# Kernel optimization log

Hardware: AMD Instinct MI355X
Metric: run time of the kernel (lower is better)

## Reference

```python
import jax, jax.numpy as jnp
import numpy as np


def setup_inputs() -> dict:
    key = jax.random.key(0)
    k1, k2 = jax.random.split(key)
    N = 16384
    NUM_ANCHORS = 64
    HIDDEN_DIM = 128
    adj = jax.random.uniform(k1, (N, N), dtype=jnp.float32)
    anchor_emb = jax.random.normal(k2, (NUM_ANCHORS, HIDDEN_DIM), dtype=jnp.float32)
    return {"adj": adj, "anchor_emb": anchor_emb}


def reference(adj, anchor_emb):
    # adj: [N, N], anchor_emb: [A, H]
    num_anchors = anchor_emb.shape[0]
    deg = jnp.sum(adj, axis=-1, keepdims=True)              # [N, 1]
    nrm = jnp.linalg.norm(deg) + 1e-6                       # scalar ||deg||_F
    # sim[:, :A] of (deg @ deg.T)/nrm computed directly without the full NxN product
    sim = (deg * deg[:num_anchors, 0][None, :]) / nrm       # [N, A]
    anchor_weights = jax.nn.softmax(sim, axis=-1)           # [N, A]
    return anchor_weights @ anchor_emb                      # [N, H]
```

## Files before the change

kernel.cpp:

```cpp
#include <hip/hip_runtime.h>


constexpr int N_NODES = 16384;
constexpr int N_ANCH  = 64;
constexpr int HID     = 128;
constexpr int ROWS_PER_BLOCK = 8;
constexpr int K1_BLOCKS = N_NODES / ROWS_PER_BLOCK;
constexpr int K3_BLOCKS = 1024;

typedef float f4 __attribute__((ext_vector_type(4)));

__global__ __launch_bounds__(256) void rowsum_kernel(const float* __restrict__ adj,
                                                     float* __restrict__ deg,
                                                     float* __restrict__ ssq_part) {
    const int t = threadIdx.x, lane = t & 63, wid = t >> 6;
    const int row0 = blockIdx.x * ROWS_PER_BLOCK + wid * 2;
    float ssq = 0.0f;

    for (int r = 0; r < 2; ++r) {
        const int row = row0 + r;
        const f4* __restrict__ p =
            reinterpret_cast<const f4*>(adj) + (size_t)row * (N_NODES / 4) + lane;
        float s = 0.0f;
        for (int c = 0; c < 4; ++c) {
            f4 v[16];
#pragma unroll
            for (int i = 0; i < 16; ++i)
                v[i] = __builtin_nontemporal_load(p + c * 1024 + i * 64);
#pragma unroll
            for (int i = 0; i < 16; ++i)
                s += (v[i].x + v[i].y) + (v[i].z + v[i].w);
        }
#pragma unroll
        for (int off = 32; off > 0; off >>= 1) s += __shfl_down(s, off, 64);
        if (lane == 0) { deg[row] = s; ssq = fmaf(s, s, ssq); }
    }

    __shared__ float sp[4];
    if (lane == 0) sp[wid] = ssq;
    __syncthreads();
    if (t == 0) ssq_part[blockIdx.x] = (sp[0] + sp[1]) + (sp[2] + sp[3]);
}

__global__ __launch_bounds__(256) void out_kernel(const float* __restrict__ deg,
                                                  const float* __restrict__ ssq_part,
                                                  const float* __restrict__ emb,
                                                  float* __restrict__ out) {
    __shared__ float s_emb[N_ANCH * HID];
    __shared__ float s_w[4][N_ANCH];
    __shared__ float s_red[4];
    __shared__ float s_inv;

    const int t = threadIdx.x, lane = t & 63, wid = t >> 6;

    float ss = 0.0f;
#pragma unroll
    for (int i = 0; i < K1_BLOCKS / 256; ++i) ss += ssq_part[t + i * 256];
#pragma unroll
    for (int off = 32; off > 0; off >>= 1) ss += __shfl_down(ss, off, 64);
    if (lane == 0) s_red[wid] = ss;

    for (int i = t; i < N_ANCH * HID / 4; i += 256)
        reinterpret_cast<f4*>(s_emb)[i] = reinterpret_cast<const f4*>(emb)[i];
    __syncthreads();
    if (t == 0)
        s_inv = 1.0f / (sqrtf((s_red[0] + s_red[1]) + (s_red[2] + s_red[3])) + 1e-6f);
    __syncthreads();
    const float inv_nrm = s_inv;

    float e0[N_ANCH], e1[N_ANCH];
#pragma unroll
    for (int a = 0; a < N_ANCH; ++a) {
        e0[a] = s_emb[a * HID + lane];
        e1[a] = s_emb[a * HID + 64 + lane];
    }

    const float da = deg[lane] * inv_nrm;
    const int row0 = (blockIdx.x * 4 + wid) * 4;

    for (int r = 0; r < 4; ++r) {
        const int row = row0 + r;
        const float sim = deg[row] * da;

        float m = sim;
#pragma unroll
        for (int off = 32; off > 0; off >>= 1) m = fmaxf(m, __shfl_xor(m, off, 64));
        const float e = __expf(sim - m);
        float sum = e;
#pragma unroll
        for (int off = 32; off > 0; off >>= 1) sum += __shfl_xor(sum, off, 64);
        s_w[wid][lane] = e / sum;

        float acc0 = 0.0f, acc1 = 0.0f;
#pragma unroll
        for (int a4 = 0; a4 < N_ANCH; a4 += 4) {
            f4 w4 = *reinterpret_cast<const f4*>(&s_w[wid][a4]);
            acc0 = fmaf(w4.x, e0[a4 + 0], acc0); acc1 = fmaf(w4.x, e1[a4 + 0], acc1);
            acc0 = fmaf(w4.y, e0[a4 + 1], acc0); acc1 = fmaf(w4.y, e1[a4 + 1], acc1);
            acc0 = fmaf(w4.z, e0[a4 + 2], acc0); acc1 = fmaf(w4.z, e1[a4 + 2], acc1);
            acc0 = fmaf(w4.w, e0[a4 + 3], acc0); acc1 = fmaf(w4.w, e1[a4 + 3], acc1);
        }
        out[(size_t)row * HID + lane]      = acc0;
        out[(size_t)row * HID + 64 + lane] = acc1;
    }
}

extern "C" void kernel_launch(void* const* d_in, const int* in_sizes, int n_in,
                              void* d_out, int out_size, void* d_ws, size_t ws_size,
                              hipStream_t stream) {
    const float* adj = (const float*)d_in[0];
    const float* emb = (const float*)d_in[1];
    float* out = (float*)d_out;

    float* deg      = (float*)d_ws;
    float* ssq_part = deg + N_NODES;

    rowsum_kernel<<<K1_BLOCKS, 256, 0, stream>>>(adj, deg, ssq_part);
    out_kernel<<<K3_BLOCKS, 256, 0, stream>>>(deg, ssq_part, emb, out);
}
```

Measured before the change: 180.7 us.

## Fuse rowsum and output kernels into one cooperative kernel with grid sync

Merges the row-sum/degree kernel and the softmax-weighted output kernel into a single cooperative launch of 512 blocks, with a grid-wide sync between the two phases. Each block now reads 32 rows of adj instead of 8, and the anchor embedding is staged into shared memory before the stream. The output phase splits work so each wave handles one 64-column half across 16 rows. This removes a kernel launch and its tail gap, at the cost of a grid barrier, fewer blocks for the bandwidth-bound adj stream, and a cooperative-launch residency requirement.

```diff
diff --git a/kernel.cpp b/kernel.cpp
--- a/kernel.cpp
+++ b/kernel.cpp
@@ -1,23 +1,36 @@
 #include <hip/hip_runtime.h>
+#include <hip/hip_cooperative_groups.h>
+
+namespace cg = cooperative_groups;
 
 
 constexpr int N_NODES = 16384;
 constexpr int N_ANCH  = 64;
 constexpr int HID     = 128;
-constexpr int ROWS_PER_BLOCK = 8;
-constexpr int K1_BLOCKS = N_NODES / ROWS_PER_BLOCK;
-constexpr int K3_BLOCKS = 1024;
+constexpr int BLOCKS  = 512;
+constexpr int RPB     = N_NODES / BLOCKS;
+constexpr int RPW     = RPB / 4;
 
 typedef float f4 __attribute__((ext_vector_type(4)));
 
-__global__ __launch_bounds__(256) void rowsum_kernel(const float* __restrict__ adj,
-                                                     float* __restrict__ deg,
-                                                     float* __restrict__ ssq_part) {
+__global__ __launch_bounds__(256, 4) void fused_kernel(const float* __restrict__ adj,
+                                                       const float* __restrict__ emb,
+                                                       float* __restrict__ out,
+                                                       float* __restrict__ deg,
+                                                       float* __restrict__ ssq_part) {
+    __shared__ float s_emb[N_ANCH * HID];
+    __shared__ float s_w[4][N_ANCH];
+    __shared__ float s_sp[4];
+    __shared__ float s_red[4];
+
     const int t = threadIdx.x, lane = t & 63, wid = t >> 6;
-    const int row0 = blockIdx.x * ROWS_PER_BLOCK + wid * 2;
+
+    for (int i = t; i < N_ANCH * HID / 4; i += 256)
+        reinterpret_cast<f4*>(s_emb)[i] = reinterpret_cast<const f4*>(emb)[i];
+
+    const int row0 = blockIdx.x * RPB + wid * RPW;
     float ssq = 0.0f;
-
-    for (int r = 0; r < 2; ++r) {
+    for (int r = 0; r < RPW; ++r) {
         const int row = row0 + r;
         const f4* __restrict__ p =
             reinterpret_cast<const f4*>(adj) + (size_t)row * (N_NODES / 4) + lane;
@@ -35,73 +48,54 @@
         for (int off = 32; off > 0; off >>= 1) s += __shfl_down(s, off, 64);
         if (lane == 0) { deg[row] = s; ssq = fmaf(s, s, ssq); }
     }
+    if (lane == 0) s_sp[wid] = ssq;
+    __syncthreads();
+    if (t == 0) ssq_part[blockIdx.x] = (s_sp[0] + s_sp[1]) + (s_sp[2] + s_sp[3]);
 
-    __shared__ float sp[4];
-    if (lane == 0) sp[wid] = ssq;
-    __syncthreads();
-    if (t == 0) ssq_part[blockIdx.x] = (sp[0] + sp[1]) + (sp[2] + sp[3]);
-}
+    cg::this_grid().sync();
 
-__global__ __launch_bounds__(256) void out_kernel(const float* __restrict__ deg,
-                                                  const float* __restrict__ ssq_part,
-                                                  const float* __restrict__ emb,
-                                                  float* __restrict__ out) {
-    __shared__ float s_emb[N_ANCH * HID];
-    __shared__ float s_w[4][N_ANCH];
-    __shared__ float s_red[4];
-    __shared__ float s_inv;
-
-    const int t = threadIdx.x, lane = t & 63, wid = t >> 6;
-
-    float ss = 0.0f;
-#pragma unroll
-    for (int i = 0; i < K1_BLOCKS / 256; ++i) ss += ssq_part[t + i * 256];
+    float ss = ssq_part[t] + ssq_part[t + 256];
 #pragma unroll
     for (int off = 32; off > 0; off >>= 1) ss += __shfl_down(ss, off, 64);
     if (lane == 0) s_red[wid] = ss;
+    __syncthreads();
+    const float inv_nrm =
+        1.0f / (sqrtf((s_red[0] + s_red[1]) + (s_red[2] + s_red[3])) + 1e-6f);
 
-    for (int i = t; i < N_ANCH * HID / 4; i += 256)
-        reinterpret_cast<f4*>(s_emb)[i] = reinterpret_cast<const f4*>(emb)[i];
-    __syncthreads();
-    if (t == 0)
-        s_inv = 1.0f / (sqrtf((s_red[0] + s_red[1]) + (s_red[2] + s_red[3])) + 1e-6f);
-    __syncthreads();
-    const float inv_nrm = s_inv;
+    const int pair = wid & 1;
+    const int half = wid >> 1;
+    const int col  = half * 64 + lane;
 
-    float e0[N_ANCH], e1[N_ANCH];
+    float e[N_ANCH];
 #pragma unroll
-    for (int a = 0; a < N_ANCH; ++a) {
-        e0[a] = s_emb[a * HID + lane];
-        e1[a] = s_emb[a * HID + 64 + lane];
-    }
+    for (int a = 0; a < N_ANCH; ++a) e[a] = s_emb[a * HID + col];
 
     const float da = deg[lane] * inv_nrm;
-    const int row0 = (blockIdx.x * 4 + wid) * 4;
+    const int rbase = blockIdx.x * RPB + pair * (RPB / 2);
 
-    for (int r = 0; r < 4; ++r) {
-        const int row = row0 + r;
+    for (int r = 0; r < RPB / 2; ++r) {
+        const int row = rbase + r;
         const float sim = deg[row] * da;
 
         float m = sim;
 #pragma unroll
         for (int off = 32; off > 0; off >>= 1) m = fmaxf(m, __shfl_xor(m, off, 64));
-        const float e = __expf(sim - m);
-        float sum = e;
+        const float ex = __expf(sim - m);
+        float sum = ex;
 #pragma unroll
         for (int off = 32; off > 0; off >>= 1) sum += __shfl_xor(sum, off, 64);
-        s_w[wid][lane] = e / sum;
+        s_w[wid][lane] = ex / sum;
 
-        float acc0 = 0.0f, acc1 = 0.0f;
+        float acc = 0.0f;
 #pragma unroll
         for (int a4 = 0; a4 < N_ANCH; a4 += 4) {
             f4 w4 = *reinterpret_cast<const f4*>(&s_w[wid][a4]);
-            acc0 = fmaf(w4.x, e0[a4 + 0], acc0); acc1 = fmaf(w4.x, e1[a4 + 0], acc1);
-            acc0 = fmaf(w4.y, e0[a4 + 1], acc0); acc1 = fmaf(w4.y, e1[a4 + 1], acc1);
-            acc0 = fmaf(w4.z, e0[a4 + 2], acc0); acc1 = fmaf(w4.z, e1[a4 + 2], acc1);
-            acc0 = fmaf(w4.w, e0[a4 + 3], acc0); acc1 = fmaf(w4.w, e1[a4 + 3], acc1);
+            acc = fmaf(w4.x, e[a4 + 0], acc);
+            acc = fmaf(w4.y, e[a4 + 1], acc);
+            acc = fmaf(w4.z, e[a4 + 2], acc);
+            acc = fmaf(w4.w, e[a4 + 3], acc);
         }
-        out[(size_t)row * HID + lane]      = acc0;
-        out[(size_t)row * HID + 64 + lane] = acc1;
+        out[(size_t)row * HID + col] = acc;
     }
 }
 
@@ -115,6 +109,7 @@
     float* deg      = (float*)d_ws;
     float* ssq_part = deg + N_NODES;
 
-    rowsum_kernel<<<K1_BLOCKS, 256, 0, stream>>>(adj, deg, ssq_part);
-    out_kernel<<<K3_BLOCKS, 256, 0, stream>>>(deg, ssq_part, emb, out);
+    void* args[] = {(void*)&adj, (void*)&emb, (void*)&out, (void*)&deg, (void*)&ssq_part};
+    hipLaunchCooperativeKernel((void*)fused_kernel, dim3(BLOCKS), dim3(256),
+                               args, 0, stream);
 }
```

Result: slower. 243.3 us (+34.6%).
